# Kernel tuning notes

Measured on AMD Instinct MI355X. Metric: run time of the kernel, lower is better.

## Reference

```python
import jax, jax.numpy as jnp
import numpy as np

N = 4096   # nodes
E = 4096   # hyperedges (== N so the original's [N,H] output is fully populated)
F = 256    # feature_size
H = 256    # hidden_size
BLOCK = 64 # node-block size for the blocked masked max/min scan


def setup_inputs() -> dict:
    key = jax.random.key(0)
    ks = jax.random.split(key, 11)
    mask = jax.random.randint(ks[4], (E, N), 0, 2, dtype=jnp.int32)
    # guarantee every hyperedge is non-empty (matches `if end > start` path)
    mask = mask.at[jnp.arange(E), jnp.arange(N)].set(1)
    s = 0.05
    return {
        "pos_features": jax.random.normal(ks[0], (N, F), jnp.float32),
        "pos_matrix": jax.random.normal(ks[1], (N, F), jnp.float32),
        "neg_features": jax.random.normal(ks[2], (N, F), jnp.float32),
        "neg_matrix": jax.random.normal(ks[3], (N, F), jnp.float32),
        "batch_mask": mask,
        "W_self": jax.random.normal(ks[5], (F, H), jnp.float32) * s,
        "b_self": jnp.zeros((H,), jnp.float32),
        "W_hyper": jax.random.normal(ks[6], (F, H), jnp.float32) * s,
        "b_hyper": jnp.zeros((H,), jnp.float32),
        "W_score": jax.random.normal(ks[7], (H, 1), jnp.float32) * s,
        "b_score": jnp.zeros((1,), jnp.float32),
    }


def maxmin_pool(mask_bool, feats):
    """Per-hyperedge (max - min) over member-node features.
    mask_bool: [E, N] bool, feats: [N, H] -> [E, H].
    Blocked over nodes to avoid materializing [E, N, H]."""
    Ee, Nn = mask_bool.shape
    Hh = feats.shape[1]
    nb = Nn // BLOCK
    mask_blocks = mask_bool.reshape(Ee, nb, BLOCK).transpose(1, 0, 2)  # [nb, E, BLOCK]
    feat_blocks = feats.reshape(nb, BLOCK, Hh)                          # [nb, BLOCK, H]

    def body(carry, xs):
        mx, mn = carry
        mblk, fblk = xs                      # [E, BLOCK], [BLOCK, H]
        m = mblk[:, :, None]                 # [E, BLOCK, 1]
        f = fblk[None]                       # [1, BLOCK, H]
        mx = jnp.maximum(mx, jnp.max(jnp.where(m, f, -jnp.inf), axis=1))
        mn = jnp.minimum(mn, jnp.min(jnp.where(m, f, jnp.inf), axis=1))
        return (mx, mn), None

    init = (jnp.full((Ee, Hh), -jnp.inf, feats.dtype),
            jnp.full((Ee, Hh), jnp.inf, feats.dtype))
    (mx, mn), _ = jax.lax.scan(body, init, (mask_blocks, feat_blocks))
    return mx - mn


def reference(pos_features, pos_matrix, neg_features, neg_matrix, batch_mask,
              W_self, b_self, W_hyper, b_hyper, W_score, b_score):
    mask = batch_mask.astype(bool)

    def branch(x_feat, x_mat):
        h = jax.nn.relu(x_feat @ W_self + b_self + x_mat @ W_hyper + b_hyper)  # [N, H]
        pooled = maxmin_pool(mask, h)                                          # [E, H]
        return jax.nn.sigmoid(pooled @ W_score + b_score)                      # [E, 1]

    pos_score = branch(pos_features, pos_matrix)
    neg_score = branch(neg_features, neg_matrix)
    return pos_score, neg_score
```

## Files before the change

### kernel.cpp

```cpp
#include <hip/hip_runtime.h>
#include <hip/hip_bf16.h>
#include <hip/hip_fp16.h>


typedef short bf16x8 __attribute__((ext_vector_type(8)));
typedef float f32x4 __attribute__((ext_vector_type(4)));
typedef short s16x2 __attribute__((ext_vector_type(2)));
typedef unsigned short u16x2 __attribute__((ext_vector_type(2)));

static __device__ __forceinline__ unsigned short f2bf(float f) {
    __hip_bfloat16 b = __float2bfloat16(f);
    return __builtin_bit_cast(unsigned short, b);
}
static __device__ __forceinline__ float f16u_to_f(unsigned u) {
    __half h = __builtin_bit_cast(__half, (unsigned short)(u & 0xffffu));
    return __half2float(h);
}
static __device__ __forceinline__ unsigned pkmax_i16(unsigned a, unsigned b) {
    s16x2 r = __builtin_elementwise_max(__builtin_bit_cast(s16x2, a), __builtin_bit_cast(s16x2, b));
    return __builtin_bit_cast(unsigned, r);
}
static __device__ __forceinline__ unsigned pkmin_u16(unsigned a, unsigned b) {
    u16x2 r = __builtin_elementwise_min(__builtin_bit_cast(u16x2, a), __builtin_bit_cast(u16x2, b));
    return __builtin_bit_cast(unsigned, r);
}

__global__ void k_prep(const int* __restrict__ mask, unsigned* __restrict__ packed,
                       const float* __restrict__ Ws, const float* __restrict__ Wh,
                       unsigned short* __restrict__ Wts, unsigned short* __restrict__ Wth) {
    const int bx = blockIdx.x, t = threadIdx.x;
    if (bx < 2048) {
        int w = bx * 256 + t;
        const int* p = mask + (size_t)w * 32;
        unsigned word = 0;
#pragma unroll
        for (int j = 0; j < 32; j += 4) {
            int4 m = *(const int4*)(p + j);
            word |= (m.x != 0 ? (1u << (31 - j)) : 0u)
                  | (m.y != 0 ? (1u << (30 - j)) : 0u)
                  | (m.z != 0 ? (1u << (29 - j)) : 0u)
                  | (m.w != 0 ? (1u << (28 - j)) : 0u);
        }
        packed[w] = word;
    } else {
        int b2 = bx - 2048;
        int k = b2 & 255, brn = b2 >> 8;
        const float* W     = brn ? Wh : Ws;
        unsigned short* Wt = brn ? Wth : Wts;
        Wt[t * 256 + k] = f2bf(W[k * 256 + t]);
    }
}

__launch_bounds__(256)
__global__ void k_gemm_relu(const float* __restrict__ pXf, const float* __restrict__ pXm,
                            const float* __restrict__ nXf, const float* __restrict__ nXm,
                            const unsigned short* __restrict__ Wts, const unsigned short* __restrict__ Wth,
                            const float* __restrict__ bs,  const float* __restrict__ bh,
                            unsigned short* __restrict__ hOut, int tmode) {
    const int t  = threadIdx.x;
    const int wv = t >> 6;
    const int l  = t & 63;
    const int lm = l & 15;
    const int q  = l >> 4;
    const int bz = blockIdx.z;
    const float* Xf = bz ? nXf : pXf;
    const float* Xm = bz ? nXm : pXm;
    unsigned short* hb = hOut + (size_t)bz * 4096 * 256;

    const int m0 = blockIdx.x * 64 + wv * 16;
    const int n0 = blockIdx.y * 64;

    f32x4 acc[4] = {};
#pragma unroll
    for (int ks = 0; ks < 512; ks += 32) {
        const float* X           = (ks < 256) ? Xf : Xm;
        const unsigned short* Wt = (ks < 256) ? Wts : Wth;
        const int kk = (ks & 255) + q * 8;
        float4 a0 = *(const float4*)(X + (m0 + lm) * 256 + kk);
        float4 a1 = *(const float4*)(X + (m0 + lm) * 256 + kk + 4);
        bf16x8 a;
        a[0] = (short)f2bf(a0.x); a[1] = (short)f2bf(a0.y);
        a[2] = (short)f2bf(a0.z); a[3] = (short)f2bf(a0.w);
        a[4] = (short)f2bf(a1.x); a[5] = (short)f2bf(a1.y);
        a[6] = (short)f2bf(a1.z); a[7] = (short)f2bf(a1.w);
#pragma unroll
        for (int nt = 0; nt < 4; nt++) {
            bf16x8 b = *(const bf16x8*)(Wt + (n0 + nt * 16 + lm) * 256 + kk);
            acc[nt] = __builtin_amdgcn_mfma_f32_16x16x32_bf16(a, b, acc[nt], 0, 0, 0);
        }
    }
    if (tmode) {
#pragma unroll
        for (int nt = 0; nt < 4; nt++) {
            const int c = n0 + nt * 16 + lm;
            const float bsum = bs[c] + bh[c];
            ushort4 v4;
#pragma unroll
            for (int i = 0; i < 4; i++) {
                float v = acc[nt][i] + bsum;
                v = v > 0.f ? v : 0.f;
                ((unsigned short*)&v4)[i] = __builtin_bit_cast(unsigned short, __float2half(v));
            }
            *(ushort4*)(hb + (size_t)c * 4096 + m0 + q * 4) = v4;
        }
    } else {
#pragma unroll
        for (int nt = 0; nt < 4; nt++) {
            const int c = n0 + nt * 16 + lm;
            const float bsum = bs[c] + bh[c];
#pragma unroll
            for (int i = 0; i < 4; i++) {
                const int r = m0 + q * 4 + i;
                float v = acc[nt][i] + bsum;
                v = v > 0.f ? v : 0.f;
                hb[(size_t)r * 256 + c] = __builtin_bit_cast(unsigned short, __float2half(v));
            }
        }
    }
}

__launch_bounds__(256)
__global__ void k_sort(const unsigned short* __restrict__ hT,
                       unsigned* __restrict__ topkG, unsigned* __restrict__ botkG) {
    __shared__ unsigned arrA[4096];
    __shared__ unsigned arrB[4096];
    __shared__ unsigned short hist[16 * 256];

    const int c = blockIdx.x, br = blockIdx.y, t = threadIdx.x;
    const int wv = t >> 6, l = t & 63;
    const unsigned short* src = hT + (size_t)(br * 256 + c) * 4096;

    {
        uint4 a = ((const uint4*)src)[t * 2];
        uint4 b = ((const uint4*)src)[t * 2 + 1];
        unsigned base = t * 16;
        unsigned w[8] = {a.x, a.y, a.z, a.w, b.x, b.y, b.z, b.w};
#pragma unroll
        for (int m = 0; m < 8; m++) {
            arrA[base + 2 * m]     = ((w[m] & 0xFFFFu) << 16) | (base + 2 * m);
            arrA[base + 2 * m + 1] = (w[m] & 0xFFFF0000u)     | (base + 2 * m + 1);
        }
    }
    __syncthreads();

    unsigned* A = arrA;
    unsigned* B = arrB;
#pragma unroll
    for (int pass = 0; pass < 4; pass++) {
        const int sh = 16 + pass * 4;
        unsigned keys[16];
        unsigned short cnt[16];
#pragma unroll
        for (int b = 0; b < 16; b++) cnt[b] = 0;
#pragma unroll
        for (int m = 0; m < 16; m++) {
            keys[m] = A[t * 16 + m];
            cnt[(keys[m] >> sh) & 15u]++;
        }
#pragma unroll
        for (int b = 0; b < 16; b++) hist[b * 256 + t] = cnt[b];
        __syncthreads();

        unsigned loc[16];
        unsigned sum = 0;
#pragma unroll
        for (int m = 0; m < 16; m++) { loc[m] = sum; sum += hist[t * 16 + m]; }
        unsigned ws = sum;
#pragma unroll
        for (int off = 1; off < 64; off <<= 1) {
            unsigned n = __shfl_up(ws, off);
            if (l >= off) ws += n;
        }
        if (l == 63) B[wv] = ws;
        __syncthreads();
        unsigned wbase = 0;
#pragma unroll
        for (int w2 = 0; w2 < 4; w2++) if (w2 < wv) wbase += B[w2];
        const unsigned ex = wbase + ws - sum;
#pragma unroll
        for (int m = 0; m < 16; m++) hist[t * 16 + m] = (unsigned short)(ex + loc[m]);
        __syncthreads();

        unsigned offs[16];
#pragma unroll
        for (int b = 0; b < 16; b++) offs[b] = hist[b * 256 + t];
#pragma unroll
        for (int m = 0; m < 16; m++) {
            unsigned b = (keys[m] >> sh) & 15u;
            B[offs[b]++] = keys[m];
        }
        __syncthreads();
        unsigned* tmp = A; A = B; B = tmp;
    }

    if (t < 64) {
        topkG[(br * 64 + t) * 256 + c] = arrA[4095 - t];
        botkG[(br * 64 + t) * 256 + c] = arrA[t];
    }
}

__launch_bounds__(256)
__global__ void k_probe(const unsigned* __restrict__ topkG,
                        const unsigned* __restrict__ botkG,
                        const unsigned* __restrict__ packed,
                        const unsigned short* __restrict__ hT,
                        const float* __restrict__ Wscore,
                        const float* __restrict__ bscore,
                        float* __restrict__ out) {
    __shared__ __align__(16) unsigned topkL[16 * 256];
    __shared__ __align__(16) unsigned botkL[16 * 256];
    __shared__ __align__(16) unsigned bitsL[16 * 128];

    const int t  = threadIdx.x;
    const int wv = t >> 6;
    const int l  = t & 63;
    const int e0 = blockIdx.x * 16;
    const int br = blockIdx.y;

    {
        const uint4* ts  = (const uint4*)(topkG + br * 16384);
        const uint4* bs2 = (const uint4*)(botkG + br * 16384);
#pragma unroll
        for (int m = 0; m < 4; m++) {
            ((uint4*)topkL)[t + m * 256] = ts[t + m * 256];
            ((uint4*)botkL)[t + m * 256] = bs2[t + m * 256];
        }
        ((uint4*)bitsL)[t]       = ((const uint4*)(packed + e0 * 128))[t];
        ((uint4*)bitsL)[t + 256] = ((const uint4*)(packed + e0 * 128))[t + 256];
    }
    __syncthreads();

    const float bsc = *bscore;
    float wsv[4];
#pragma unroll
    for (int sl = 0; sl < 4; sl++) wsv[sl] = Wscore[l + 64 * sl];

#pragma unroll 1
    for (int k = 0; k < 4; k++) {
        const int e = wv * 4 + k;
        const unsigned* mk = &bitsL[e * 128];
        float s = 0.f;
#pragma unroll
        for (int sl = 0; sl < 4; sl++) {
            const int c = l + 64 * sl;

            unsigned sel = 0xFFFFFFFFu;
#pragma unroll 1
            for (int g = 0; g < 2; g++) {
                unsigned kk[8]; int ss[8];
#pragma unroll
                for (int j = 0; j < 8; j++) kk[j] = topkL[(g * 8 + j) * 256 + c];
#pragma unroll
                for (int j = 0; j < 8; j++)
                    ss[j] = (int)(mk[(kk[j] & 4095u) >> 5] << (kk[j] & 31u));
                unsigned fnd = 0xFFFFFFFFu;
#pragma unroll
                for (int j = 7; j >= 0; j--) if (ss[j] < 0) fnd = kk[j];
                if (fnd != 0xFFFFFFFFu) { sel = fnd; break; }
            }
            if (sel == 0xFFFFFFFFu) {
                const unsigned* tg = topkG + br * 16384 + c;
#pragma unroll 1
                for (int p = 16; p < 64; p++) {
                    unsigned key = tg[p * 256];
                    if ((int)(mk[(key & 4095u) >> 5] << (key & 31u)) < 0) { sel = key; break; }
                }
            }
            if (sel == 0xFFFFFFFFu) {
                const unsigned short* col = hT + (size_t)(br * 256 + c) * 4096;
                unsigned best = 0;
#pragma unroll 1
                for (int n = 0; n < 4096; n++)
                    if ((int)(mk[n >> 5] << (n & 31)) < 0) { unsigned v = col[n]; if (v > best) best = v; }
                sel = best << 16;
            }
            const float vmax = f16u_to_f(sel >> 16);

            sel = 0xFFFFFFFFu;
#pragma unroll 1
            for (int g = 0; g < 2; g++) {
                unsigned kk[8]; int ss[8];
#pragma unroll
                for (int j = 0; j < 8; j++) kk[j] = botkL[(g * 8 + j) * 256 + c];
#pragma unroll
                for (int j = 0; j < 8; j++)
                    ss[j] = (int)(mk[(kk[j] & 4095u) >> 5] << (kk[j] & 31u));
                unsigned fnd = 0xFFFFFFFFu;
#pragma unroll
                for (int j = 7; j >= 0; j--) if (ss[j] < 0) fnd = kk[j];
                if (fnd != 0xFFFFFFFFu) { sel = fnd; break; }
            }
            if (sel == 0xFFFFFFFFu) {
                const unsigned* bg = botkG + br * 16384 + c;
#pragma unroll 1
                for (int p = 16; p < 64; p++) {
                    unsigned key = bg[p * 256];
                    if ((int)(mk[(key & 4095u) >> 5] << (key & 31u)) < 0) { sel = key; break; }
                }
            }
            if (sel == 0xFFFFFFFFu) {
                const unsigned short* col = hT + (size_t)(br * 256 + c) * 4096;
                unsigned best = 0xFFFFu;
#pragma unroll 1
                for (int n = 0; n < 4096; n++)
                    if ((int)(mk[n >> 5] << (n & 31)) < 0) { unsigned v = col[n]; if (v < best) best = v; }
                sel = best << 16;
            }
            const float vmin = f16u_to_f(sel >> 16);

            s += (vmax - vmin) * wsv[sl];
        }
#pragma unroll
        for (int off = 32; off; off >>= 1) s += __shfl_xor(s, off);
        if (l == 0)
            out[br * 4096 + e0 + e] = 1.f / (1.f + __expf(-(s + bsc)));
    }
}

#define POOL_STEP(WE, MX0, MX1, MN0, MN1, VX, VY)                          \
    {                                                                      \
        asm("s_add_u32 %[we], %[we], %[we]\n\t"                            \
            "s_cbranch_scc0 Lskip%=\n\t"                                   \
            "v_pk_max_i16 %[mx0], %[mx0], %[vx]\n\t"                       \
            "v_pk_max_i16 %[mx1], %[mx1], %[vy]\n\t"                       \
            "v_pk_min_u16 %[mn0], %[mn0], %[vx]\n\t"                       \
            "v_pk_min_u16 %[mn1], %[mn1], %[vy]\n"                         \
            "Lskip%=:"                                                     \
            : [we] "+s"(WE),                                               \
              [mx0] "+v"(MX0), [mx1] "+v"(MX1),                            \
              [mn0] "+v"(MN0), [mn1] "+v"(MN1)                             \
            : [vx] "v"(VX), [vy] "v"(VY)                                   \
            : "scc");                                                      \
    }

__launch_bounds__(512, 8)
__global__ void k_pool9(const unsigned short* __restrict__ hAll,
                        const unsigned* __restrict__ packed,
                        const float* __restrict__ Wscore,
                        const float* __restrict__ bscore,
                        float* __restrict__ out) {
    __shared__ __align__(16) unsigned bits[4 * 128];
    __shared__ __align__(16) unsigned part[8][4][64][4];

    const int t  = threadIdx.x;
    const int wv = t >> 6;
    const int l  = t & 63;
    const int e0 = blockIdx.x * 4;
    const int br = blockIdx.y;
    const unsigned short* h = hAll + (size_t)br * 4096 * 256;

    if (t < 128) ((uint4*)bits)[t] = ((const uint4*)(packed + e0 * 128))[t];
    __syncthreads();

    unsigned mx0[4], mx1[4], mn0[4], mn1[4];
#pragma unroll
    for (int e = 0; e < 4; e++) {
        mx0[e] = 0x80008000u; mx1[e] = 0x80008000u;
        mn0[e] = 0xFFFFFFFFu; mn1[e] = 0xFFFFFFFFu;
    }

#pragma unroll 1
    for (int ch = 0; ch < 16; ch++) {
        const int w0 = wv * 16 + ch;
        unsigned we0 = (unsigned)__builtin_amdgcn_readfirstlane((int)bits[0 * 128 + w0]);
        unsigned we1 = (unsigned)__builtin_amdgcn_readfirstlane((int)bits[1 * 128 + w0]);
        unsigned we2 = (unsigned)__builtin_amdgcn_readfirstlane((int)bits[2 * 128 + w0]);
        unsigned we3 = (unsigned)__builtin_amdgcn_readfirstlane((int)bits[3 * 128 + w0]);

        const unsigned short* hp = h + (size_t)(wv * 512 + ch * 32) * 256 + 4 * l;
#pragma unroll
        for (int jj = 0; jj < 8; jj++) {
            uint2 v0 = *(const uint2*)(hp + (jj * 4 + 0) * 256);
            uint2 v1 = *(const uint2*)(hp + (jj * 4 + 1) * 256);
            uint2 v2 = *(const uint2*)(hp + (jj * 4 + 2) * 256);
            uint2 v3 = *(const uint2*)(hp + (jj * 4 + 3) * 256);

            POOL_STEP(we0, mx0[0], mx1[0], mn0[0], mn1[0], v0.x, v0.y);
            POOL_STEP(we1, mx0[1], mx1[1], mn0[1], mn1[1], v0.x, v0.y);
            POOL_STEP(we2, mx0[2], mx1[2], mn0[2], mn1[2], v0.x, v0.y);
            POOL_STEP(we3, mx0[3], mx1[3], mn0[3], mn1[3], v0.x, v0.y);
            POOL_STEP(we0, mx0[0], mx1[0], mn0[0], mn1[0], v1.x, v1.y);
            POOL_STEP(we1, mx0[1], mx1[1], mn0[1], mn1[1], v1.x, v1.y);
            POOL_STEP(we2, mx0[2], mx1[2], mn0[2], mn1[2], v1.x, v1.y);
            POOL_STEP(we3, mx0[3], mx1[3], mn0[3], mn1[3], v1.x, v1.y);
            POOL_STEP(we0, mx0[0], mx1[0], mn0[0], mn1[0], v2.x, v2.y);
            POOL_STEP(we1, mx0[1], mx1[1], mn0[1], mn1[1], v2.x, v2.y);
            POOL_STEP(we2, mx0[2], mx1[2], mn0[2], mn1[2], v2.x, v2.y);
            POOL_STEP(we3, mx0[3], mx1[3], mn0[3], mn1[3], v2.x, v2.y);
            POOL_STEP(we0, mx0[0], mx1[0], mn0[0], mn1[0], v3.x, v3.y);
            POOL_STEP(we1, mx0[1], mx1[1], mn0[1], mn1[1], v3.x, v3.y);
            POOL_STEP(we2, mx0[2], mx1[2], mn0[2], mn1[2], v3.x, v3.y);
            POOL_STEP(we3, mx0[3], mx1[3], mn0[3], mn1[3], v3.x, v3.y);
        }
    }

#pragma unroll
    for (int e = 0; e < 4; e++) {
        uint4 p; p.x = mx0[e]; p.y = mx1[e]; p.z = mn0[e]; p.w = mn1[e];
        *(uint4*)&part[wv][e][l][0] = p;
    }
    __syncthreads();

    if (wv < 4) {
        unsigned rmx0 = 0x80008000u, rmx1 = 0x80008000u;
        unsigned rmn0 = 0xFFFFFFFFu, rmn1 = 0xFFFFFFFFu;
#pragma unroll
        for (int w2 = 0; w2 < 8; w2++) {
            uint4 p = *(const uint4*)&part[w2][wv][l][0];
            rmx0 = pkmax_i16(rmx0, p.x);  rmx1 = pkmax_i16(rmx1, p.y);
            rmn0 = pkmin_u16(rmn0, p.z);  rmn1 = pkmin_u16(rmn1, p.w);
        }
        float4 wsv = *(const float4*)(Wscore + 4 * l);
        const float bsc = *bscore;
        float s = (f16u_to_f(rmx0)       - f16u_to_f(rmn0))       * wsv.x
                + (f16u_to_f(rmx0 >> 16) - f16u_to_f(rmn0 >> 16)) * wsv.y
                + (f16u_to_f(rmx1)       - f16u_to_f(rmn1))       * wsv.z
                + (f16u_to_f(rmx1 >> 16) - f16u_to_f(rmn1 >> 16)) * wsv.w;
#pragma unroll
        for (int off = 32; off; off >>= 1) s += __shfl_xor(s, off);
        if (l == 0)
            out[br * 4096 + e0 + wv] = 1.f / (1.f + __expf(-(s + bsc)));
    }
}

extern "C" void kernel_launch(void* const* d_in, const int* in_sizes, int n_in,
                              void* d_out, int out_size, void* d_ws, size_t ws_size,
                              hipStream_t stream) {
    const float* pf  = (const float*)d_in[0];
    const float* pm  = (const float*)d_in[1];
    const float* nf  = (const float*)d_in[2];
    const float* nm  = (const float*)d_in[3];
    const int*   msk = (const int*)d_in[4];
    const float* Wsf = (const float*)d_in[5];
    const float* bsf = (const float*)d_in[6];
    const float* Whp = (const float*)d_in[7];
    const float* bhp = (const float*)d_in[8];
    const float* Wsc = (const float*)d_in[9];
    const float* bsc = (const float*)d_in[10];
    float* out = (float*)d_out;

    char* ws = (char*)d_ws;
    const size_t MB = 1024u * 1024u;
    unsigned short* hbuf  = (unsigned short*)(ws);
    unsigned*       pck   = (unsigned*)(ws + 4 * MB);
    unsigned short* Wts   = (unsigned short*)(ws + 6 * MB);
    unsigned short* Wth   = Wts + 256 * 256;
    unsigned*       topkG = (unsigned*)(ws + 6 * MB + 256 * 1024);
    unsigned*       botkG = (unsigned*)(ws + 6 * MB + 384 * 1024);
    const size_t need = 6 * MB + 512 * 1024;

    k_prep<<<2560, 256, 0, stream>>>(msk, pck, Wsf, Whp, Wts, Wth);

    if (ws_size >= need) {
        k_gemm_relu<<<dim3(64, 4, 2), 256, 0, stream>>>(pf, pm, nf, nm, Wts, Wth, bsf, bhp, hbuf, 1);
        k_sort<<<dim3(256, 2), 256, 0, stream>>>(hbuf, topkG, botkG);
        k_probe<<<dim3(256, 2), 256, 0, stream>>>(topkG, botkG, pck, hbuf, Wsc, bsc, out);
    } else {
        k_gemm_relu<<<dim3(64, 4, 2), 256, 0, stream>>>(pf, pm, nf, nm, Wts, Wth, bsf, bhp, hbuf, 0);
        k_pool9<<<dim3(1024, 2), 512, 0, stream>>>(hbuf, pck, Wsc, bsc, out);
    }
}
```

Before: 189.6 us.

## Fuse mask bit-packing into sort kernel and tile weight transpose through LDS

Mask packing moves out of the prep kernel and into the sort kernel. Each sort thread loads 128 mask ints and packs them into four words, with the loads spread across the first radix passes so memory latency hides behind sort work. The weight transpose becomes a separate small kernel that uses an LDS tile, so both reads and writes are coalesced. This is meant to remove the serial 64MB mask-read pass from the critical path, at the cost of register pressure in the sort kernel.

```diff
diff --git a/kernel.cpp b/kernel.cpp
--- a/kernel.cpp
+++ b/kernel.cpp
@@ -25,30 +25,39 @@
     return __builtin_bit_cast(unsigned, r);
 }
 
-__global__ void k_prep(const int* __restrict__ mask, unsigned* __restrict__ packed,
-                       const float* __restrict__ Ws, const float* __restrict__ Wh,
-                       unsigned short* __restrict__ Wts, unsigned short* __restrict__ Wth) {
-    const int bx = blockIdx.x, t = threadIdx.x;
-    if (bx < 2048) {
-        int w = bx * 256 + t;
-        const int* p = mask + (size_t)w * 32;
-        unsigned word = 0;
-#pragma unroll
-        for (int j = 0; j < 32; j += 4) {
-            int4 m = *(const int4*)(p + j);
-            word |= (m.x != 0 ? (1u << (31 - j)) : 0u)
-                  | (m.y != 0 ? (1u << (30 - j)) : 0u)
-                  | (m.z != 0 ? (1u << (29 - j)) : 0u)
-                  | (m.w != 0 ? (1u << (28 - j)) : 0u);
-        }
-        packed[w] = word;
-    } else {
-        int b2 = bx - 2048;
-        int k = b2 & 255, brn = b2 >> 8;
-        const float* W     = brn ? Wh : Ws;
-        unsigned short* Wt = brn ? Wth : Wts;
-        Wt[t * 256 + k] = f2bf(W[k * 256 + t]);
-    }
+__global__ void k_prepW(const float* __restrict__ Ws, const float* __restrict__ Wh,
+                        unsigned short* __restrict__ Wts, unsigned short* __restrict__ Wth) {
+    __shared__ unsigned short tile[64][65];
+    const int k0 = blockIdx.x * 64, n0 = blockIdx.y * 64;
+    const float* W     = blockIdx.z ? Wh : Ws;
+    unsigned short* Wt = blockIdx.z ? Wth : Wts;
+    const int t = threadIdx.x;
+#pragma unroll
+    for (int m = 0; m < 16; m++) {
+        int li = t + m * 256; int r = li >> 6, c = li & 63;
+        tile[r][c] = f2bf(W[(size_t)(k0 + r) * 256 + n0 + c]);
+    }
+    __syncthreads();
+#pragma unroll
+    for (int m = 0; m < 16; m++) {
+        int li = t + m * 256; int c2 = li >> 6, r2 = li & 63;
+        Wt[(size_t)(n0 + c2) * 256 + k0 + r2] = tile[r2][c2];
+    }
+}
+
+__global__ void k_pack(const int* __restrict__ mask, unsigned* __restrict__ packed) {
+    const int w = blockIdx.x * 256 + threadIdx.x;
+    const int* p = mask + (size_t)w * 32;
+    unsigned word = 0;
+#pragma unroll
+    for (int j = 0; j < 32; j += 4) {
+        int4 m = *(const int4*)(p + j);
+        word |= (m.x != 0 ? (1u << (31 - j)) : 0u)
+              | (m.y != 0 ? (1u << (30 - j)) : 0u)
+              | (m.z != 0 ? (1u << (29 - j)) : 0u)
+              | (m.w != 0 ? (1u << (28 - j)) : 0u);
+    }
+    packed[w] = word;
 }
 
 __launch_bounds__(256)
@@ -120,8 +129,10 @@
 }
 
 __launch_bounds__(256)
-__global__ void k_sort(const unsigned short* __restrict__ hT,
-                       unsigned* __restrict__ topkG, unsigned* __restrict__ botkG) {
+__global__ void k_sortpack(const unsigned short* __restrict__ hT,
+                           const int* __restrict__ mask,
+                           unsigned* __restrict__ packed,
+                           unsigned* __restrict__ topkG, unsigned* __restrict__ botkG) {
     __shared__ unsigned arrA[4096];
     __shared__ unsigned arrB[4096];
     __shared__ unsigned short hist[16 * 256];
@@ -129,6 +140,12 @@
     const int c = blockIdx.x, br = blockIdx.y, t = threadIdx.x;
     const int wv = t >> 6, l = t & 63;
     const unsigned short* src = hT + (size_t)(br * 256 + c) * 4096;
+
+    const int gtid = (br * 256 + c) * 256 + t;
+    const int4* mp = (const int4*)(mask + (size_t)gtid * 128);
+    int4 mr[16];
+#pragma unroll
+    for (int i = 0; i < 16; i++) mr[i] = mp[i];
 
     {
         uint4 a = ((const uint4*)src)[t * 2];
@@ -143,11 +160,27 @@
     }
     __syncthreads();
 
+    unsigned pw[4];
+#pragma unroll
+    for (int m = 0; m < 2; m++) {
+        unsigned word = 0;
+#pragma unroll
+        for (int j2 = 0; j2 < 8; j2++) {
+            int4 v = mr[m * 8 + j2];
+            const int j = j2 * 4;
+            word |= (v.x != 0 ? (1u << (31 - j)) : 0u)
+                  | (v.y != 0 ? (1u << (30 - j)) : 0u)
+                  | (v.z != 0 ? (1u << (29 - j)) : 0u)
+                  | (v.w != 0 ? (1u << (28 - j)) : 0u);
+        }
+        pw[m] = word;
+    }
+#pragma unroll
+    for (int i = 0; i < 16; i++) mr[i] = mp[16 + i];
+
     unsigned* A = arrA;
     unsigned* B = arrB;
-#pragma unroll
-    for (int pass = 0; pass < 4; pass++) {
-        const int sh = 16 + pass * 4;
+    auto do_pass = [&](int sh) {
         unsigned keys[16];
         unsigned short cnt[16];
 #pragma unroll
@@ -191,12 +224,32 @@
         }
         __syncthreads();
         unsigned* tmp = A; A = B; B = tmp;
-    }
+    };
+
+    do_pass(16);
+#pragma unroll
+    for (int m = 0; m < 2; m++) {
+        unsigned word = 0;
+#pragma unroll
+        for (int j2 = 0; j2 < 8; j2++) {
+            int4 v = mr[m * 8 + j2];
+            const int j = j2 * 4;
+            word |= (v.x != 0 ? (1u << (31 - j)) : 0u)
+                  | (v.y != 0 ? (1u << (30 - j)) : 0u)
+                  | (v.z != 0 ? (1u << (29 - j)) : 0u)
+                  | (v.w != 0 ? (1u << (28 - j)) : 0u);
+        }
+        pw[2 + m] = word;
+    }
+    do_pass(20);
+    do_pass(24);
+    do_pass(28);
 
     if (t < 64) {
         topkG[(br * 64 + t) * 256 + c] = arrA[4095 - t];
         botkG[(br * 64 + t) * 256 + c] = arrA[t];
     }
+    *(uint4*)(packed + (size_t)gtid * 4) = make_uint4(pw[0], pw[1], pw[2], pw[3]);
 }
 
 __launch_bounds__(256)
@@ -449,13 +502,14 @@
     unsigned*       botkG = (unsigned*)(ws + 6 * MB + 384 * 1024);
     const size_t need = 6 * MB + 512 * 1024;
 
-    k_prep<<<2560, 256, 0, stream>>>(msk, pck, Wsf, Whp, Wts, Wth);
+    k_prepW<<<dim3(4, 4, 2), 256, 0, stream>>>(Wsf, Whp, Wts, Wth);
 
     if (ws_size >= need) {
         k_gemm_relu<<<dim3(64, 4, 2), 256, 0, stream>>>(pf, pm, nf, nm, Wts, Wth, bsf, bhp, hbuf, 1);
-        k_sort<<<dim3(256, 2), 256, 0, stream>>>(hbuf, topkG, botkG);
+        k_sortpack<<<dim3(256, 2), 256, 0, stream>>>(hbuf, msk, pck, topkG, botkG);
         k_probe<<<dim3(256, 2), 256, 0, stream>>>(topkG, botkG, pck, hbuf, Wsc, bsc, out);
     } else {
+        k_pack<<<2048, 256, 0, stream>>>(msk, pck);
         k_gemm_relu<<<dim3(64, 4, 2), 256, 0, stream>>>(pf, pm, nf, nm, Wts, Wth, bsf, bhp, hbuf, 0);
         k_pool9<<<dim3(1024, 2), 512, 0, stream>>>(hbuf, pck, Wsc, bsc, out);
     }
```

Result: no change. 188.6 us (-0.6%).
